# Kernel tuning notes

Measured on AMD Instinct MI355X. Metric: run time of the kernel, lower is better.

## Reference

```python
import jax, jax.numpy as jnp
import numpy as np

B, CIN, IMG, PATCH = 4, 1, 64, 8
SIDE = IMG // PATCH            # 8
N = SIDE ** 3                  # 512 tokens
C = 384
HEADS, HD = 6, 64
IFF = 1536
WS, SHIFT = 2, 1
NB = 4                         # 4 dense blocks + 4 shifted-window blocks (8 layers)
NKP = 15
EPS = 1e-5


def _ln(x, g, b):
    m = x.mean(-1, keepdims=True)
    v = ((x - m) ** 2).mean(-1, keepdims=True)
    return (x - m) * jax.lax.rsqrt(v + EPS) * g + b


def _mhsa(x, qw, kw, vw, pw, pb):
    # per-head Q/K/V linears (no bias), stacked as [H, C, HD]
    q = jnp.einsum('bnc,hcd->bhnd', x, qw)
    k = jnp.einsum('bnc,hcd->bhnd', x, kw)
    v = jnp.einsum('bnc,hcd->bhnd', x, vw)
    a = jax.nn.softmax(jnp.einsum('bhnd,bhmd->bhnm', q, k) / np.float32(np.sqrt(HD)), axis=-1)
    o = jnp.einsum('bhnm,bhmd->bhnd', a, v)
    o = o.transpose(0, 2, 1, 3).reshape(x.shape[0], x.shape[1], C)
    return o @ pw + pb


def _swin_attn(x, qkv_w, qkv_b, pw, pb):
    Bn = x.shape[0]
    H = W = D = SIDE
    xv = x.transpose(0, 2, 1).reshape(Bn, C, H, W, D)
    xv = jnp.roll(xv, (-SHIFT, -SHIFT, -SHIFT), axis=(2, 3, 4))
    # window partition -> [Bn*nw^3, WS^3, C]
    xv = xv.reshape(Bn, C, H // WS, WS, W // WS, WS, D // WS, WS)
    win = xv.transpose(0, 2, 4, 6, 3, 5, 7, 1).reshape(-1, WS ** 3, C)
    qkv = win @ qkv_w + qkv_b                                      # [Bw, ws3, 3C]
    qkv = qkv.reshape(win.shape[0], WS ** 3, 3, HEADS, HD).transpose(2, 0, 3, 1, 4)
    q, k, v = qkv[0], qkv[1], qkv[2]
    a = jax.nn.softmax(jnp.einsum('whnd,whmd->whnm', q, k) / np.float32(np.sqrt(HD)), axis=-1)
    o = jnp.einsum('whnm,whmd->whnd', a, v)
    o = o.transpose(0, 2, 1, 3).reshape(win.shape[0], WS ** 3, C)
    o = o @ pw + pb
    # window reverse
    o = o.reshape(Bn, H // WS, W // WS, D // WS, WS, WS, WS, C)
    o = o.transpose(0, 7, 1, 4, 2, 5, 3, 6).reshape(Bn, C, H, W, D)
    o = jnp.roll(o, (SHIFT, SHIFT, SHIFT), axis=(2, 3, 4))
    return o.reshape(Bn, C, -1).transpose(0, 2, 1)


def _ffn(x, w1, b1, w2, b2):
    return jax.nn.relu(x @ w1 + b1) @ w2 + b2


def _deconv2(x, w, b):
    # ConvTranspose3d kernel=stride=2 (no overlap): pure block upsample GEMM
    Bn, Cc, H, W, D = x.shape
    O = w.shape[1]
    y = jnp.einsum('bchwd,coijk->bohiwjdk', x, w)
    return y.reshape(Bn, O, 2 * H, 2 * W, 2 * D) + b[None, :, None, None, None]


def _bn_relu(x, g, b, m, v):
    sh = (1, -1, 1, 1, 1)
    y = (x - m.reshape(sh)) * jax.lax.rsqrt(v.reshape(sh) + EPS) * g.reshape(sh) + b.reshape(sh)
    return jax.nn.relu(y)


def setup_inputs() -> dict:
    key = jax.random.key(0)
    ks = iter(jax.random.split(key, 40))
    nrm = lambda shape, s=0.02: jax.random.normal(next(ks), shape, jnp.float32) * s
    inp = {
        'x': jax.random.normal(next(ks), (B, CIN, IMG, IMG, IMG), jnp.float32),
        'patch_w': nrm((C, CIN, PATCH, PATCH, PATCH)),
        'patch_b': jnp.zeros((C,), jnp.float32),
        'pos_emb': nrm((1, N, C)),
        # 4 dense blocks (stacked)
        'm_ln1_g': jnp.ones((NB, C)), 'm_ln1_b': jnp.zeros((NB, C)),
        'm_qw': nrm((NB, HEADS, C, HD)), 'm_kw': nrm((NB, HEADS, C, HD)), 'm_vw': nrm((NB, HEADS, C, HD)),
        'm_proj_w': nrm((NB, C, C)), 'm_proj_b': jnp.zeros((NB, C)),
        'm_ln2_g': jnp.ones((NB, C)), 'm_ln2_b': jnp.zeros((NB, C)),
        'm_w1': nrm((NB, C, IFF)), 'm_b1': jnp.zeros((NB, IFF)),
        'm_w2': nrm((NB, IFF, C)), 'm_b2': jnp.zeros((NB, C)),
        # 4 shifted-window blocks (stacked)
        's_ln1_g': jnp.ones((NB, C)), 's_ln1_b': jnp.zeros((NB, C)),
        's_qkv_w': nrm((NB, C, 3 * C)), 's_qkv_b': jnp.zeros((NB, 3 * C)),
        's_proj_w': nrm((NB, C, C)), 's_proj_b': jnp.zeros((NB, C)),
        's_ln2_g': jnp.ones((NB, C)), 's_ln2_b': jnp.zeros((NB, C)),
        's_w1': nrm((NB, C, IFF)), 's_b1': jnp.zeros((NB, IFF)),
        's_w2': nrm((NB, IFF, C)), 's_b2': jnp.zeros((NB, C)),
        # ClassicDecoder
        'd1_w': nrm((C, C, 2, 2, 2)), 'd1_b': jnp.zeros((C,)),
        'bn1_g': jnp.ones((C,)), 'bn1_b': jnp.zeros((C,)), 'bn1_m': jnp.zeros((C,)), 'bn1_v': jnp.ones((C,)),
        'd2_w': nrm((C, C, 2, 2, 2)), 'd2_b': jnp.zeros((C,)),
        'bn2_g': jnp.ones((C,)), 'bn2_b': jnp.zeros((C,)), 'bn2_m': jnp.zeros((C,)), 'bn2_v': jnp.ones((C,)),
        'out_w': nrm((NKP, C)), 'out_b': jnp.zeros((NKP,)),
    }
    return inp


def reference(x, patch_w, patch_b, pos_emb,
              m_ln1_g, m_ln1_b, m_qw, m_kw, m_vw, m_proj_w, m_proj_b,
              m_ln2_g, m_ln2_b, m_w1, m_b1, m_w2, m_b2,
              s_ln1_g, s_ln1_b, s_qkv_w, s_qkv_b, s_proj_w, s_proj_b,
              s_ln2_g, s_ln2_b, s_w1, s_b1, s_w2, s_b2,
              d1_w, d1_b, bn1_g, bn1_b, bn1_m, bn1_v,
              d2_w, d2_b, bn2_g, bn2_b, bn2_m, bn2_v,
              out_w, out_b):
    # patch embedding: Conv3d(k=stride=patch) -> [B, N, C]
    t = jax.lax.conv_general_dilated(x, patch_w, (PATCH, PATCH, PATCH), 'VALID',
                                     dimension_numbers=('NCDHW', 'OIDHW', 'NCDHW'))
    t = t + patch_b[None, :, None, None, None]
    t = t.reshape(B, C, N).transpose(0, 2, 1) + pos_emb
    for i in range(2 * NB):
        j = i // 2
        if i % 2 == 0:  # dense Block
            t = t + _mhsa(_ln(t, m_ln1_g[j], m_ln1_b[j]), m_qw[j], m_kw[j], m_vw[j], m_proj_w[j], m_proj_b[j])
            t = t + _ffn(_ln(t, m_ln2_g[j], m_ln2_b[j]), m_w1[j], m_b1[j], m_w2[j], m_b2[j])
        else:           # ShiftedWindowBlock
            t = t + _swin_attn(_ln(t, s_ln1_g[j], s_ln1_b[j]), s_qkv_w[j], s_qkv_b[j], s_proj_w[j], s_proj_b[j])
            t = t + _ffn(_ln(t, s_ln2_g[j], s_ln2_b[j]), s_w1[j], s_b1[j], s_w2[j], s_b2[j])
    # ClassicDecoder
    y = t.transpose(0, 2, 1).reshape(B, C, SIDE, SIDE, SIDE)
    y = _bn_relu(_deconv2(y, d1_w, d1_b), bn1_g, bn1_b, bn1_m, bn1_v)
    y = _bn_relu(_deconv2(y, d2_w, d2_b), bn2_g, bn2_b, bn2_m, bn2_v)
    y = jnp.einsum('bchwd,oc->bohwd', y, out_w) + out_b[None, :, None, None, None]
    return y
```

## Files before the change

kernel.cpp:

```cpp
#include <hip/hip_runtime.h>
#include <hip/hip_bf16.h>


typedef unsigned short u16;
typedef __bf16 bf16x8 __attribute__((ext_vector_type(8)));
typedef float f32x4 __attribute__((ext_vector_type(4)));

__device__ __forceinline__ u16 f2bf(float f) {
  unsigned u = __builtin_bit_cast(unsigned, f);
  return (u16)((u + 0x7FFFu + ((u >> 16) & 1u)) >> 16);
}
__device__ __forceinline__ float bf2f(u16 b) {
  unsigned u = ((unsigned)b) << 16;
  return __builtin_bit_cast(float, u);
}

#define GLOAD_LDS16(g, l)                                                      \
  __builtin_amdgcn_global_load_lds(                                            \
      (const __attribute__((address_space(1))) unsigned int*)(const void*)(g), \
      (__attribute__((address_space(3))) unsigned int*)(void*)(l), 16, 0, 0)

struct MmP {
  const u16* A;
  const u16* Bt;
  const float* bias;
  void* C;
  void* aux;
  const float* e1; const float* e2; const float* e3; const float* e4;
  int K, ZH, lda, ldb, ldc;
  long aSb, aSh, bSb, bSh, cSb, cSh;
};

template<int MODE, int BM>
__global__ __launch_bounds__(256) void mfma_gemm(MmP p) {
  const int z = blockIdx.z;
  const int zb = z / p.ZH, zh = z - zb * p.ZH;
  const u16* A  = p.A  + zb * p.aSb + zh * p.aSh;
  const u16* Bt = p.Bt + zb * p.bSb + zh * p.bSh;
  const int m0 = blockIdx.y * BM, n0 = blockIdx.x * 64;

  __shared__ u16 As[2][BM * 64];
  __shared__ u16 Bs[2][64 * 64];

  const int tid = threadIdx.x;
  const int wid = tid >> 6, lane = tid & 63;
  constexpr int MI = BM / 32;
  const int wm = (wid >> 1) * (BM / 2), wn = (wid & 1) * 32;
  const int lr = lane & 15, lg = lane >> 4;
  constexpr int ACH = BM / 32;

  f32x4 acc[MI][2];
  #pragma unroll
  for (int i = 0; i < MI; i++)
    #pragma unroll
    for (int j = 0; j < 2; j++) acc[i][j] = (f32x4){0.f, 0.f, 0.f, 0.f};

  auto stage = [&](int buf, int kt) {
    #pragma unroll
    for (int i = 0; i < ACH; i++) {
      int c = i * 256 + tid;
      int row = c >> 3, cc = c & 7;
      int gk = ((cc ^ (row & 7)) << 3) + (kt << 6);
      GLOAD_LDS16(A + (long)(m0 + row) * p.lda + gk, As[buf] + c * 8);
    }
    #pragma unroll
    for (int i = 0; i < 2; i++) {
      int c = i * 256 + tid;
      int row = c >> 3, cc = c & 7;
      int gk = ((cc ^ (row & 7)) << 3) + (kt << 6);
      GLOAD_LDS16(Bt + (long)(n0 + row) * p.ldb + gk, Bs[buf] + c * 8);
    }
  };

  const int nKT = p.K >> 6;
  stage(0, 0);
  asm volatile("s_waitcnt vmcnt(0)");
  __syncthreads();

  int cur = 0;
  for (int kt = 0; kt < nKT; ++kt) {
    const bool more = (kt + 1 < nKT);
    if (more) stage(cur ^ 1, kt + 1);

    bf16x8 af[MI][2], bfr[2][2];
    #pragma unroll
    for (int i = 0; i < MI; i++)
      #pragma unroll
      for (int ks = 0; ks < 2; ks++) {
        int row = wm + i * 16 + lr;
        int j = ks * 4 + lg;
        af[i][ks] = *(const bf16x8*)(As[cur] + (row * 8 + (j ^ (row & 7))) * 8);
      }
    #pragma unroll
    for (int jn = 0; jn < 2; jn++)
      #pragma unroll
      for (int ks = 0; ks < 2; ks++) {
        int row = wn + jn * 16 + lr;
        int j = ks * 4 + lg;
        bfr[jn][ks] = *(const bf16x8*)(Bs[cur] + (row * 8 + (j ^ (row & 7))) * 8);
      }
    #pragma unroll
    for (int i = 0; i < MI; i++)
      #pragma unroll
      for (int jn = 0; jn < 2; jn++)
        #pragma unroll
        for (int ks = 0; ks < 2; ks++)
          acc[i][jn] = __builtin_amdgcn_mfma_f32_16x16x32_bf16(
              af[i][ks], bfr[jn][ks], acc[i][jn], 0, 0, 0);

    if (more) {
      asm volatile("s_waitcnt vmcnt(0)");
      __syncthreads();
      cur ^= 1;
    }
  }

  const long coff = zb * p.cSb + zh * p.cSh;
  #pragma unroll
  for (int i = 0; i < MI; i++) {
    const int rowb = m0 + wm + i * 16 + lg * 4;
    #pragma unroll
    for (int jn = 0; jn < 2; jn++) {
      const int col = n0 + wn + jn * 16 + lr;
      const float bv = p.bias ? p.bias[col] : 0.f;
      #pragma unroll
      for (int r = 0; r < 4; r++) {
        const int row = rowb + r;
        const float v = acc[i][jn][r];
        if constexpr (MODE == 0) {
          ((u16*)p.C)[coff + (long)row * p.ldc + col] = f2bf(v + bv);
        } else if constexpr (MODE == 1) {
          ((float*)p.C)[coff + (long)row * p.ldc + col] =
              v + bv + p.e1[(long)(row & 511) * 384 + col];
        } else if constexpr (MODE == 2) {
          ((float*)p.C)[coff + (long)row * p.ldc + col] += v + bv;
        } else if constexpr (MODE == 3) {
          ((u16*)p.C)[coff + (long)row * p.ldc + col] = f2bf(fmaxf(v + bv, 0.f));
        } else if constexpr (MODE == 5) {
          float raw = v + bv;
          float val = fmaxf((raw - p.e3[col]) * rsqrtf(p.e4[col] + 1e-5f) * p.e1[col] + p.e2[col], 0.f);
          int b = row >> 9, hwd = row & 511;
          int h = hwd >> 6, w = (hwd >> 3) & 7, d = hwd & 7;
          int i_ = zh >> 2, j_ = (zh >> 1) & 1, k_ = zh & 1;
          long tokn = (long)b * 4096 + (2 * h + i_) * 256 + (2 * w + j_) * 16 + (2 * d + k_);
          ((u16*)p.C)[tokn * 384 + col] = f2bf(val);
        } else if constexpr (MODE == 6) {
          float raw = v + bv;
          float val = fmaxf((raw - p.e3[col]) * rsqrtf(p.e4[col] + 1e-5f) * p.e1[col] + p.e2[col], 0.f);
          ((u16*)p.C)[(long)row * p.ldc + col] = f2bf(val);
        } else if constexpr (MODE == 7) {
          u16 bv16 = f2bf(v);
          ((u16*)p.C)[coff + (long)row * p.ldc + col] = bv16;
          if (col >= 768) {
            int bb = row >> 9, tt = row & 511;
            int hh = (col - 768) >> 6, dd = col & 63;
            ((u16*)p.aux)[(((long)bb * 6 + hh) << 15) + (dd << 9) + tt] = bv16;
          }
        }
      }
    }
  }
}

__global__ __launch_bounds__(512) void attnsm_k(const u16* __restrict__ qkv, u16* __restrict__ P) {
  const int bh = blockIdx.y;
  const int b = bh / 6, h = bh - b * 6;
  const int qt = blockIdx.x;
  const int tid = threadIdx.x, wid = tid >> 6, lane = tid & 63;
  const int lr = lane & 15, lg = lane >> 4;
  __shared__ u16 Ks[512 * 64];
  const u16* qbase = qkv + ((long)b * 512) * 1152 + h * 64;

  #pragma unroll
  for (int i = 0; i < 8; i++) {
    int c = i * 512 + tid;
    int t = c >> 3, cc = c & 7;
    int gk = (cc ^ (t & 7)) << 3;
    GLOAD_LDS16(qbase + (long)t * 1152 + 384 + gk, Ks + c * 8);
  }
  const int qrow = qt * 128 + wid * 16 + lr;
  bf16x8 qf[2];
  #pragma unroll
  for (int ks = 0; ks < 2; ks++)
    qf[ks] = *(const bf16x8*)(qbase + (long)qrow * 1152 + (ks * 4 + lg) * 8);
  asm volatile("s_waitcnt vmcnt(0)");
  __syncthreads();

  f32x4 s[32];
  #pragma unroll
  for (int nt = 0; nt < 32; nt++) {
    s[nt] = (f32x4){0.f, 0.f, 0.f, 0.f};
    #pragma unroll
    for (int ks = 0; ks < 2; ks++) {
      int row = nt * 16 + lr;
      int j = ks * 4 + lg;
      bf16x8 kf = *(const bf16x8*)(Ks + (row * 8 + (j ^ (row & 7))) * 8);
      s[nt] = __builtin_amdgcn_mfma_f32_16x16x32_bf16(qf[ks], kf, s[nt], 0, 0, 0);
    }
  }
  float mx[4] = {-1e30f, -1e30f, -1e30f, -1e30f};
  #pragma unroll
  for (int nt = 0; nt < 32; nt++)
    #pragma unroll
    for (int r = 0; r < 4; r++) { s[nt][r] *= 0.125f; mx[r] = fmaxf(mx[r], s[nt][r]); }
  #pragma unroll
  for (int o = 8; o >= 1; o >>= 1)
    #pragma unroll
    for (int r = 0; r < 4; r++) mx[r] = fmaxf(mx[r], __shfl_xor(mx[r], o));
  float sum[4] = {0.f, 0.f, 0.f, 0.f};
  #pragma unroll
  for (int nt = 0; nt < 32; nt++)
    #pragma unroll
    for (int r = 0; r < 4; r++) { float e = __expf(s[nt][r] - mx[r]); s[nt][r] = e; sum[r] += e; }
  #pragma unroll
  for (int o = 8; o >= 1; o >>= 1)
    #pragma unroll
    for (int r = 0; r < 4; r++) sum[r] += __shfl_xor(sum[r], o);
  float inv[4];
  #pragma unroll
  for (int r = 0; r < 4; r++) inv[r] = 1.f / sum[r];

  u16* Pb = P + (long)bh * 262144;
  const int prow0 = qt * 128 + wid * 16 + lg * 4;
  #pragma unroll
  for (int nt = 0; nt < 32; nt++)
    #pragma unroll
    for (int r = 0; r < 4; r++)
      Pb[(long)(prow0 + r) * 512 + nt * 16 + lr] = f2bf(s[nt][r] * inv[r]);
}


__global__ __launch_bounds__(256) void ln_k(const float* __restrict__ x, const float* __restrict__ g,
                                            const float* __restrict__ b, u16* __restrict__ y) {
  const int row = (blockIdx.x << 2) + (threadIdx.x >> 6);
  const int lane = threadIdx.x & 63;
  const float* xr = x + (long)row * 384;
  float v[6]; float s = 0.f;
  #pragma unroll
  for (int i = 0; i < 6; i++) { v[i] = xr[lane + (i << 6)]; s += v[i]; }
  #pragma unroll
  for (int o = 32; o >= 1; o >>= 1) s += __shfl_xor(s, o);
  const float mean = s * (1.f / 384.f);
  float q = 0.f;
  #pragma unroll
  for (int i = 0; i < 6; i++) { float dd = v[i] - mean; q += dd * dd; }
  #pragma unroll
  for (int o = 32; o >= 1; o >>= 1) q += __shfl_xor(q, o);
  const float rstd = rsqrtf(q * (1.f / 384.f) + 1e-5f);
  u16* yr = y + (long)row * 384;
  #pragma unroll
  for (int i = 0; i < 6; i++) {
    int c = lane + (i << 6);
    yr[c] = f2bf((v[i] - mean) * rstd * g[c] + b[c]);
  }
}

__global__ __launch_bounds__(64) void swin_k(const u16* __restrict__ qkv, u16* __restrict__ attno) {
  const int blk = blockIdx.x;
  const int h = blk % 6; const int bw = blk / 6;
  const int b = bw >> 6, win = bw & 63;
  const int wh = win >> 4, ww = (win >> 2) & 3, wd = win & 3;
  const int lane = threadIdx.x;
  __shared__ float qs[8][68], ks[8][68], vs[8][68], attw[8][8];
  __shared__ int ntok[8];
  if (lane < 8) {
    int i = lane >> 2, j = (lane >> 1) & 1, k = lane & 1;
    int oh = (2 * wh + i + 1) & 7, ow = (2 * ww + j + 1) & 7, od = (2 * wd + k + 1) & 7;
    ntok[lane] = oh * 64 + ow * 8 + od;
  }
  __syncthreads();
  #pragma unroll
  for (int t = 0; t < 8; t++) {
    long base = ((long)b * 512 + ntok[t]) * 1152 + h * 64 + lane;
    qs[t][lane] = bf2f(qkv[base]);
    ks[t][lane] = bf2f(qkv[base + 384]);
    vs[t][lane] = bf2f(qkv[base + 768]);
  }
  __syncthreads();
  const int tq = lane >> 3, tm = lane & 7;
  float sc = 0.f;
  #pragma unroll 16
  for (int d = 0; d < 64; d++) sc += qs[tq][d] * ks[tm][d];
  sc *= 0.125f;
  float mx = sc;
  mx = fmaxf(mx, __shfl_xor(mx, 4));
  mx = fmaxf(mx, __shfl_xor(mx, 2));
  mx = fmaxf(mx, __shfl_xor(mx, 1));
  float e = __expf(sc - mx);
  float sm = e;
  sm += __shfl_xor(sm, 4); sm += __shfl_xor(sm, 2); sm += __shfl_xor(sm, 1);
  attw[tq][tm] = e / sm;
  __syncthreads();
  #pragma unroll
  for (int t = 0; t < 8; t++) {
    float o = 0.f;
    #pragma unroll
    for (int m = 0; m < 8; m++) o += attw[t][m] * vs[m][lane];
    attno[((long)b * 512 + ntok[t]) * 384 + h * 64 + lane] = f2bf(o);
  }
}

__global__ __launch_bounds__(256) void im2col_k(const float* __restrict__ x, u16* __restrict__ xp) {
  const int i = blockIdx.x * 256 + threadIdx.x;
  const int l = i & 511; const int m = i >> 9;
  const int b = m >> 9, n = m & 511;
  const int h = n >> 6, w = (n >> 3) & 7, d = n & 7;
  const int pi = l >> 6, pj = (l >> 3) & 7, pk = l & 7;
  xp[i] = f2bf(x[(long)b * 262144 + (long)(h * 8 + pi) * 4096 + (w * 8 + pj) * 64 + (d * 8 + pk)]);
}

__global__ __launch_bounds__(256) void castw_k(const float* __restrict__ in, u16* __restrict__ out, int n) {
  for (int i = blockIdx.x * 256 + threadIdx.x; i < n; i += gridDim.x * 256)
    out[i] = f2bf(in[i]);
}

struct TJ { const float* s[7]; u16* d[7]; };
__global__ __launch_bounds__(256) void transpose_tiled_k(TJ tj) {
  __shared__ u16 tile[64][65];
  const int cumt[8] = {0, 432, 576, 720, 1296, 1872, 2448, 3024};
  const int bi = blockIdx.x;
  int j = 0;
  #pragma unroll
  for (int t = 1; t < 7; t++) if (bi >= cumt[t]) j = t;
  const int li = bi - cumt[j];
  const int Kj = (j >= 5) ? 1536 : 384;
  const int Nj = (j == 0) ? 1152 : ((j == 3 || j == 4) ? 1536 : 384);
  const int tn_cnt = Nj >> 6;
  const int per_z = (Kj >> 6) * tn_cnt;
  const int z = li / per_z;
  int rem = li - z * per_z;
  const int tk = rem / tn_cnt, tn = rem - tk * tn_cnt;
  const float* src = tj.s[j] + (long)z * Kj * Nj;
  u16* dst = tj.d[j] + (long)z * Kj * Nj;
  const int k0 = tk << 6, n0 = tn << 6;
  const int rl = threadIdx.x >> 6, c = threadIdx.x & 63;
  #pragma unroll
  for (int i = 0; i < 16; i++) {
    int r = i * 4 + rl;
    tile[r][c] = f2bf(src[(long)(k0 + r) * Nj + n0 + c]);
  }
  __syncthreads();
  #pragma unroll
  for (int i = 0; i < 16; i++) {
    int n = i * 4 + rl;
    dst[(long)(n0 + n) * Kj + k0 + c] = tile[c][n];
  }
}

__global__ __launch_bounds__(256) void repack_mqkv_k2(const float* __restrict__ qw, const float* __restrict__ kw,
                                                      const float* __restrict__ vw, u16* __restrict__ out) {
  __shared__ u16 tile[64][65];
  const int bi = blockIdx.x;
  const int j = bi / 108;
  int rem = bi - j * 108;
  const int s = rem / 36; rem -= s * 36;
  const int h = rem / 6, tk = rem - h * 6;
  const float* src = (s == 0 ? qw : s == 1 ? kw : vw) + (long)j * 147456;
  const int rl = threadIdx.x >> 6, cc = threadIdx.x & 63;
  #pragma unroll
  for (int i = 0; i < 16; i++) {
    int cl = tk * 64 + i * 4 + rl;
    tile[i * 4 + rl][cc] = f2bf(src[(long)(h * 384 + cl) * 64 + cc]);
  }
  __syncthreads();
  u16* ob = out + (long)j * 442368 + (long)(s * 384 + h * 64) * 384 + tk * 64;
  #pragma unroll
  for (int i = 0; i < 16; i++) {
    int d = i * 4 + rl;
    ob[(long)d * 384 + cc] = tile[cc][d];
  }
}

__global__ __launch_bounds__(256) void repack_dw_k2(const float* __restrict__ in, u16* __restrict__ out) {
  __shared__ u16 ds[32][514];
  const int bo = blockIdx.x % 6, bc = blockIdx.x / 6;
  const int c0 = bc * 32, o0 = bo * 64;
  #pragma unroll 4
  for (int it = 0; it < 64; it++) {
    int fl = it * 256 + threadIdx.x;
    int cr = fl >> 9, mm = fl & 511;
    ds[cr][mm] = f2bf(in[(long)(c0 + cr) * 3072 + o0 * 8 + mm]);
  }
  __syncthreads();
  #pragma unroll 4
  for (int it = 0; it < 64; it++) {
    int fl = it * 256 + threadIdx.x;
    int ijk = fl >> 11, rem = fl & 2047;
    int oo = rem >> 5, cr = rem & 31;
    out[(long)ijk * 147456 + (long)(o0 + oo) * 384 + c0 + cr] = ds[cr][oo * 8 + ijk];
  }
}

__global__ __launch_bounds__(256) void contract_k(const u16* __restrict__ act, const float* __restrict__ ow,
                                                  const float* __restrict__ ob, float* __restrict__ out, int ijk) {
  __shared__ __align__(16) float tile[16][388];
  __shared__ __align__(16) float wsh[15][388];
  const int tid = threadIdx.x;
  for (int idx = tid; idx < 15 * 384; idx += 256) {
    int kp = idx / 384, c = idx - kp * 384;
    wsh[kp][c] = ow[idx];
  }
  const long row0 = (long)blockIdx.x << 4;
  for (int idx = tid; idx < 16 * 384; idx += 256) {
    int r = idx / 384, c = idx - r * 384;
    tile[r][c] = bf2f(act[(row0 + r) * 384 + c]);
  }
  __syncthreads();
  const int r = tid >> 4, kp = tid & 15;
  if (kp < 15) {
    float acc = 0.f;
    #pragma unroll 8
    for (int c = 0; c < 384; c += 4) {
      float4 a = *(const float4*)&tile[r][c];
      float4 w = *(const float4*)&wsh[kp][c];
      acc += a.x * w.x + a.y * w.y + a.z * w.z + a.w * w.w;
    }
    const int gm = (int)row0 + r;
    const int b = gm >> 12, h = (gm >> 8) & 15, w = (gm >> 4) & 15, d = gm & 15;
    const int i = ijk >> 2, j = (ijk >> 1) & 1, k = ijk & 1;
    const long o = ((long)(b * 15 + kp) << 15) + (2 * h + i) * 1024 + (2 * w + j) * 32 + (2 * d + k);
    out[o] = acc + ob[kp];
  }
}


static MmP mk(const u16* A, const u16* Bt, const float* bias, void* C,
              int K, int lda, int ldb, int ldc) {
  MmP p{};
  p.A = A; p.Bt = Bt; p.bias = bias; p.C = C; p.aux = nullptr;
  p.e1 = p.e2 = p.e3 = p.e4 = nullptr;
  p.K = K; p.ZH = 1; p.lda = lda; p.ldb = ldb; p.ldc = ldc;
  p.aSb = p.aSh = p.bSb = p.bSh = p.cSb = p.cSh = 0;
  return p;
}

extern "C" void kernel_launch(void* const* d_in, const int* in_sizes, int n_in,
                              void* d_out, int out_size, void* d_ws, size_t ws_size,
                              hipStream_t stream) {
  (void)in_sizes; (void)n_in; (void)out_size; (void)ws_size;
  const float* x        = (const float*)d_in[0];
  const float* patch_w  = (const float*)d_in[1];
  const float* patch_b  = (const float*)d_in[2];
  const float* pos_emb  = (const float*)d_in[3];
  const float* m_ln1_g  = (const float*)d_in[4];
  const float* m_ln1_b  = (const float*)d_in[5];
  const float* m_qw     = (const float*)d_in[6];
  const float* m_kw     = (const float*)d_in[7];
  const float* m_vw     = (const float*)d_in[8];
  const float* m_proj_w = (const float*)d_in[9];
  const float* m_proj_b = (const float*)d_in[10];
  const float* m_ln2_g  = (const float*)d_in[11];
  const float* m_ln2_b  = (const float*)d_in[12];
  const float* m_w1     = (const float*)d_in[13];
  const float* m_b1     = (const float*)d_in[14];
  const float* m_w2     = (const float*)d_in[15];
  const float* m_b2     = (const float*)d_in[16];
  const float* s_ln1_g  = (const float*)d_in[17];
  const float* s_ln1_b  = (const float*)d_in[18];
  const float* s_qkv_w  = (const float*)d_in[19];
  const float* s_qkv_b  = (const float*)d_in[20];
  const float* s_proj_w = (const float*)d_in[21];
  const float* s_proj_b = (const float*)d_in[22];
  const float* s_ln2_g  = (const float*)d_in[23];
  const float* s_ln2_b  = (const float*)d_in[24];
  const float* s_w1     = (const float*)d_in[25];
  const float* s_b1     = (const float*)d_in[26];
  const float* s_w2     = (const float*)d_in[27];
  const float* s_b2     = (const float*)d_in[28];
  const float* d1_w     = (const float*)d_in[29];
  const float* d1_b     = (const float*)d_in[30];
  const float* bn1_g    = (const float*)d_in[31];
  const float* bn1_b    = (const float*)d_in[32];
  const float* bn1_m    = (const float*)d_in[33];
  const float* bn1_v    = (const float*)d_in[34];
  const float* d2_w     = (const float*)d_in[35];
  const float* d2_b     = (const float*)d_in[36];
  const float* bn2_g    = (const float*)d_in[37];
  const float* bn2_b    = (const float*)d_in[38];
  const float* bn2_m    = (const float*)d_in[39];
  const float* bn2_v    = (const float*)d_in[40];
  const float* out_w    = (const float*)d_in[41];
  const float* out_b    = (const float*)d_in[42];
  float* out = (float*)d_out;

  char* wsp = (char*)d_ws;
  auto alloc = [&](size_t bytes) { void* p = wsp; wsp += (bytes + 255) & ~(size_t)255; return p; };
  float* tok    = (float*)alloc(786432 * 4);
  u16* wqkv_m   = (u16*)alloc(1769472 * 2);
  u16* wqkv_s   = (u16*)alloc(1769472 * 2);
  u16* wproj_m  = (u16*)alloc(589824 * 2);
  u16* wproj_s  = (u16*)alloc(589824 * 2);
  u16* w1m      = (u16*)alloc(2359296 * 2);
  u16* w1s      = (u16*)alloc(2359296 * 2);
  u16* w2m      = (u16*)alloc(2359296 * 2);
  u16* w2s      = (u16*)alloc(2359296 * 2);
  u16* wpatch   = (u16*)alloc(196608 * 2);
  u16* wd1      = (u16*)alloc(1179648 * 2);
  u16* wd2      = (u16*)alloc(1179648 * 2);
  u16* lnb      = (u16*)alloc(786432 * 2);
  u16* qkvb     = (u16*)alloc(2359296 * 2);
  u16* attnob   = (u16*)alloc(786432 * 2);
  u16* ffnhb    = (u16*)alloc(3145728 * 2);
  u16* scoresb  = (u16*)alloc(6291456 * 2);
  u16* vTb      = (u16*)alloc(786432 * 2);
  u16* xpb   = scoresb;
  u16* y1b   = scoresb;
  u16* out2b = qkvb;
  u16* tokb  = vTb;

  castw_k<<<256, 256, 0, stream>>>(patch_w, wpatch, 196608);
  repack_mqkv_k2<<<432, 256, 0, stream>>>(m_qw, m_kw, m_vw, wqkv_m);
  {
    TJ tj;
    tj.s[0] = s_qkv_w;  tj.d[0] = wqkv_s;
    tj.s[1] = m_proj_w; tj.d[1] = wproj_m;
    tj.s[2] = s_proj_w; tj.d[2] = wproj_s;
    tj.s[3] = m_w1;     tj.d[3] = w1m;
    tj.s[4] = s_w1;     tj.d[4] = w1s;
    tj.s[5] = m_w2;     tj.d[5] = w2m;
    tj.s[6] = s_w2;     tj.d[6] = w2s;
    transpose_tiled_k<<<3024, 256, 0, stream>>>(tj);
  }
  repack_dw_k2<<<72, 256, 0, stream>>>(d1_w, wd1);
  repack_dw_k2<<<72, 256, 0, stream>>>(d2_w, wd2);

  im2col_k<<<4096, 256, 0, stream>>>(x, xpb);
  {
    MmP p = mk(xpb, wpatch, patch_b, tok, 512, 512, 512, 384);
    p.e1 = pos_emb;
    mfma_gemm<1, 64><<<dim3(6, 32, 1), 256, 0, stream>>>(p);
  }

  for (int j = 0; j < 4; j++) {
    ln_k<<<512, 256, 0, stream>>>(tok, m_ln1_g + j * 384, m_ln1_b + j * 384, lnb);
    {
      MmP p = mk(lnb, wqkv_m + (long)j * 442368, nullptr, qkvb, 384, 384, 384, 1152);
      p.aux = vTb;
      mfma_gemm<7, 128><<<dim3(18, 16, 1), 256, 0, stream>>>(p);
    }
    attnsm_k<<<dim3(4, 24, 1), 512, 0, stream>>>(qkvb, scoresb);
    {
      MmP p = mk(scoresb, vTb, nullptr, attnob, 512, 512, 512, 384);
      p.ZH = 6; p.aSb = 1572864; p.aSh = 262144; p.bSb = 196608; p.bSh = 32768;
      p.cSb = 196608; p.cSh = 64;
      mfma_gemm<0, 64><<<dim3(1, 8, 24), 256, 0, stream>>>(p);
    }
    {
      MmP p = mk(attnob, wproj_m + (long)j * 147456, m_proj_b + j * 384, tok, 384, 384, 384, 384);
      mfma_gemm<2, 64><<<dim3(6, 32, 1), 256, 0, stream>>>(p);
    }
    ln_k<<<512, 256, 0, stream>>>(tok, m_ln2_g + j * 384, m_ln2_b + j * 384, lnb);
    {
      MmP p = mk(lnb, w1m + (long)j * 589824, m_b1 + j * 1536, ffnhb, 384, 384, 384, 1536);
      mfma_gemm<3, 128><<<dim3(24, 16, 1), 256, 0, stream>>>(p);
    }
    {
      MmP p = mk(ffnhb, w2m + (long)j * 589824, m_b2 + j * 384, tok, 1536, 1536, 1536, 384);
      mfma_gemm<2, 64><<<dim3(6, 32, 1), 256, 0, stream>>>(p);
    }

    ln_k<<<512, 256, 0, stream>>>(tok, s_ln1_g + j * 384, s_ln1_b + j * 384, lnb);
    {
      MmP p = mk(lnb, wqkv_s + (long)j * 442368, s_qkv_b + j * 1152, qkvb, 384, 384, 384, 1152);
      mfma_gemm<0, 128><<<dim3(18, 16, 1), 256, 0, stream>>>(p);
    }
    swin_k<<<1536, 64, 0, stream>>>(qkvb, attnob);
    {
      MmP p = mk(attnob, wproj_s + (long)j * 147456, s_proj_b + j * 384, tok, 384, 384, 384, 384);
      mfma_gemm<2, 64><<<dim3(6, 32, 1), 256, 0, stream>>>(p);
    }
    ln_k<<<512, 256, 0, stream>>>(tok, s_ln2_g + j * 384, s_ln2_b + j * 384, lnb);
    {
      MmP p = mk(lnb, w1s + (long)j * 589824, s_b1 + j * 1536, ffnhb, 384, 384, 384, 1536);
      mfma_gemm<3, 128><<<dim3(24, 16, 1), 256, 0, stream>>>(p);
    }
    {
      MmP p = mk(ffnhb, w2s + (long)j * 589824, s_b2 + j * 384, tok, 1536, 1536, 1536, 384);
      mfma_gemm<2, 64><<<dim3(6, 32, 1), 256, 0, stream>>>(p);
    }
  }

  castw_k<<<768, 256, 0, stream>>>(tok, tokb, 786432);
  {
    MmP p = mk(tokb, wd1, d1_b, y1b, 384, 384, 384, 384);
    p.ZH = 8; p.bSh = 147456;
    p.e1 = bn1_g; p.e2 = bn1_b; p.e3 = bn1_m; p.e4 = bn1_v;
    mfma_gemm<5, 128><<<dim3(6, 16, 8), 256, 0, stream>>>(p);
  }
  for (int ijk = 0; ijk < 8; ijk++) {
    {
      MmP p = mk(y1b, wd2 + (long)ijk * 147456, d2_b, out2b, 384, 384, 384, 384);
      p.e1 = bn2_g; p.e2 = bn2_b; p.e3 = bn2_m; p.e4 = bn2_v;
      mfma_gemm<6, 128><<<dim3(6, 128, 1), 256, 0, stream>>>(p);
    }
    contract_k<<<1024, 256, 0, stream>>>(out2b, out_w, out_b, out, ijk);
  }
}
```

Measured before the change: 1.066 ms.

## Fuse second deconv GEMM, BN-ReLU and output projection into one kernel

Replaces the per-offset loop of deconv2 GEMM plus a separate 1x1 output contraction with a single kernel covering all eight offsets. Each 64-row tile runs the MFMA GEMM, applies bias, BN and ReLU, keeps the bf16 result in LDS and contracts it with the 15-channel output weights directly. This removes 16 launches and the round trip of the large intermediate activation through global memory, at the cost of heavy LDS use per block. It also shrinks the attention softmax block to 256 threads with twice as many blocks, and merges the two decoder weight repack launches.

```diff
diff --git a/kernel.cpp b/kernel.cpp
--- a/kernel.cpp
+++ b/kernel.cpp
@@ -4,6 +4,7 @@
 
 typedef unsigned short u16;
 typedef __bf16 bf16x8 __attribute__((ext_vector_type(8)));
+typedef unsigned short u16x8 __attribute__((ext_vector_type(8)));
 typedef float f32x4 __attribute__((ext_vector_type(4)));
 
 __device__ __forceinline__ u16 f2bf(float f) {
@@ -144,10 +145,6 @@
           int i_ = zh >> 2, j_ = (zh >> 1) & 1, k_ = zh & 1;
           long tokn = (long)b * 4096 + (2 * h + i_) * 256 + (2 * w + j_) * 16 + (2 * d + k_);
           ((u16*)p.C)[tokn * 384 + col] = f2bf(val);
-        } else if constexpr (MODE == 6) {
-          float raw = v + bv;
-          float val = fmaxf((raw - p.e3[col]) * rsqrtf(p.e4[col] + 1e-5f) * p.e1[col] + p.e2[col], 0.f);
-          ((u16*)p.C)[(long)row * p.ldc + col] = f2bf(val);
         } else if constexpr (MODE == 7) {
           u16 bv16 = f2bf(v);
           ((u16*)p.C)[coff + (long)row * p.ldc + col] = bv16;
@@ -162,7 +159,131 @@
   }
 }
 
-__global__ __launch_bounds__(512) void attnsm_k(const u16* __restrict__ qkv, u16* __restrict__ P) {
+__global__ __launch_bounds__(512) void dc2_k(const u16* __restrict__ y1, const u16* __restrict__ wd2,
+                                             const float* __restrict__ d2b,
+                                             const float* __restrict__ g, const float* __restrict__ bta,
+                                             const float* __restrict__ mu, const float* __restrict__ var,
+                                             const float* __restrict__ ow, const float* __restrict__ ob,
+                                             float* __restrict__ out) {
+  __shared__ char smem[114688];
+  u16* As = (u16*)smem;
+  u16* Bs = (u16*)(smem + 16384);
+  u16* H2 = (u16*)(smem + 16384);
+  float* ows = (float*)(smem + 16384 + 50176);
+
+  const int ijk = blockIdx.y;
+  const int m0 = blockIdx.x * 64;
+  const u16* Bt = wd2 + (long)ijk * 147456;
+  const int tid = threadIdx.x;
+  const int wid = tid >> 6, lane = tid & 63;
+  const int wr = wid >> 2, wc = wid & 3;
+  const int lr = lane & 15, lg = lane >> 4;
+
+  f32x4 acc[2][6];
+  #pragma unroll
+  for (int i = 0; i < 2; i++)
+    #pragma unroll
+    for (int j = 0; j < 6; j++) acc[i][j] = (f32x4){0.f, 0.f, 0.f, 0.f};
+
+  auto stage = [&](int buf, int kt) {
+    {
+      int c = tid;
+      int row = c >> 3, cc = c & 7;
+      int gk = ((cc ^ (row & 7)) << 3) + (kt << 6);
+      GLOAD_LDS16(y1 + (long)(m0 + row) * 384 + gk, As + buf * 4096 + c * 8);
+    }
+    #pragma unroll
+    for (int i = 0; i < 6; i++) {
+      int c = i * 512 + tid;
+      int row = c >> 3, cc = c & 7;
+      int gk = ((cc ^ (row & 7)) << 3) + (kt << 6);
+      GLOAD_LDS16(Bt + (long)row * 384 + gk, Bs + buf * 24576 + c * 8);
+    }
+  };
+  stage(0, 0);
+  asm volatile("s_waitcnt vmcnt(0)");
+  __syncthreads();
+  int cur = 0;
+  for (int kt = 0; kt < 6; ++kt) {
+    const bool more = (kt < 5);
+    if (more) stage(cur ^ 1, kt + 1);
+    bf16x8 af[2][2], bfr[6][2];
+    #pragma unroll
+    for (int i = 0; i < 2; i++)
+      #pragma unroll
+      for (int ks = 0; ks < 2; ks++) {
+        int row = wr * 32 + i * 16 + lr;
+        int j = ks * 4 + lg;
+        af[i][ks] = *(const bf16x8*)(As + cur * 4096 + (row * 8 + (j ^ (row & 7))) * 8);
+      }
+    #pragma unroll
+    for (int jn = 0; jn < 6; jn++)
+      #pragma unroll
+      for (int ks = 0; ks < 2; ks++) {
+        int row = wc * 96 + jn * 16 + lr;
+        int j = ks * 4 + lg;
+        bfr[jn][ks] = *(const bf16x8*)(Bs + cur * 24576 + (row * 8 + (j ^ (row & 7))) * 8);
+      }
+    #pragma unroll
+    for (int i = 0; i < 2; i++)
+      #pragma unroll
+      for (int jn = 0; jn < 6; jn++)
+        #pragma unroll
+        for (int ks = 0; ks < 2; ks++)
+          acc[i][jn] = __builtin_amdgcn_mfma_f32_16x16x32_bf16(
+              af[i][ks], bfr[jn][ks], acc[i][jn], 0, 0, 0);
+    if (more) {
+      asm volatile("s_waitcnt vmcnt(0)");
+      __syncthreads();
+      cur ^= 1;
+    }
+  }
+  __syncthreads();
+
+  #pragma unroll
+  for (int i = 0; i < 2; i++)
+    #pragma unroll
+    for (int jn = 0; jn < 6; jn++) {
+      const int col = wc * 96 + jn * 16 + lr;
+      const float scale = rsqrtf(var[col] + 1e-5f) * g[col];
+      const float bias2 = bta[col] - mu[col] * scale;
+      const float db = d2b[col];
+      #pragma unroll
+      for (int r = 0; r < 4; r++) {
+        int row = wr * 32 + i * 16 + lg * 4 + r;
+        float val = fmaxf((acc[i][jn][r] + db) * scale + bias2, 0.f);
+        H2[row * 392 + col] = f2bf(val);
+      }
+    }
+  for (int idx = tid; idx < 15 * 384; idx += 512) {
+    int kp = idx / 384, c = idx - kp * 384;
+    ows[kp * 388 + c] = ow[idx];
+  }
+  __syncthreads();
+
+  const int kp = tid & 15, rbase = tid >> 4;
+  if (kp < 15) {
+    const int i_ = ijk >> 2, j_ = (ijk >> 1) & 1, k_ = ijk & 1;
+    #pragma unroll
+    for (int pass = 0; pass < 2; pass++) {
+      const int r = rbase + pass * 32;
+      float a = 0.f;
+      #pragma unroll 4
+      for (int c = 0; c < 384; c += 8) {
+        u16x8 hv = *(const u16x8*)&H2[r * 392 + c];
+        const float* wp = &ows[kp * 388 + c];
+        #pragma unroll
+        for (int u = 0; u < 8; u++) a += bf2f(hv[u]) * wp[u];
+      }
+      const int gm = m0 + r;
+      const int b = gm >> 12, h = (gm >> 8) & 15, w = (gm >> 4) & 15, d = gm & 15;
+      const long o = ((long)(b * 15 + kp) << 15) + (2 * h + i_) * 1024 + (2 * w + j_) * 32 + (2 * d + k_);
+      out[o] = a + ob[kp];
+    }
+  }
+}
+
+__global__ __launch_bounds__(256) void attnsm_k(const u16* __restrict__ qkv, u16* __restrict__ P) {
   const int bh = blockIdx.y;
   const int b = bh / 6, h = bh - b * 6;
   const int qt = blockIdx.x;
@@ -172,13 +293,13 @@
   const u16* qbase = qkv + ((long)b * 512) * 1152 + h * 64;
 
   #pragma unroll
-  for (int i = 0; i < 8; i++) {
-    int c = i * 512 + tid;
+  for (int i = 0; i < 16; i++) {
+    int c = i * 256 + tid;
     int t = c >> 3, cc = c & 7;
     int gk = (cc ^ (t & 7)) << 3;
     GLOAD_LDS16(qbase + (long)t * 1152 + 384 + gk, Ks + c * 8);
   }
-  const int qrow = qt * 128 + wid * 16 + lr;
+  const int qrow = qt * 64 + wid * 16 + lr;
   bf16x8 qf[2];
   #pragma unroll
   for (int ks = 0; ks < 2; ks++)
@@ -221,7 +342,7 @@
   for (int r = 0; r < 4; r++) inv[r] = 1.f / sum[r];
 
   u16* Pb = P + (long)bh * 262144;
-  const int prow0 = qt * 128 + wid * 16 + lg * 4;
+  const int prow0 = qt * 64 + wid * 16 + lg * 4;
   #pragma unroll
   for (int nt = 0; nt < 32; nt++)
     #pragma unroll
@@ -371,9 +492,14 @@
   }
 }
 
-__global__ __launch_bounds__(256) void repack_dw_k2(const float* __restrict__ in, u16* __restrict__ out) {
+__global__ __launch_bounds__(256) void repack_dw2_k(const float* __restrict__ in1, u16* __restrict__ out1,
+                                                    const float* __restrict__ in2, u16* __restrict__ out2) {
   __shared__ u16 ds[32][514];
-  const int bo = blockIdx.x % 6, bc = blockIdx.x / 6;
+  const int sel = blockIdx.x >= 72;
+  const float* in = sel ? in2 : in1;
+  u16* out = sel ? out2 : out1;
+  const int bx = sel ? blockIdx.x - 72 : blockIdx.x;
+  const int bo = bx % 6, bc = bx / 6;
   const int c0 = bc * 32, o0 = bo * 64;
   #pragma unroll 4
   for (int it = 0; it < 64; it++) {
@@ -388,38 +514,6 @@
     int ijk = fl >> 11, rem = fl & 2047;
     int oo = rem >> 5, cr = rem & 31;
     out[(long)ijk * 147456 + (long)(o0 + oo) * 384 + c0 + cr] = ds[cr][oo * 8 + ijk];
-  }
-}
-
-__global__ __launch_bounds__(256) void contract_k(const u16* __restrict__ act, const float* __restrict__ ow,
-                                                  const float* __restrict__ ob, float* __restrict__ out, int ijk) {
-  __shared__ __align__(16) float tile[16][388];
-  __shared__ __align__(16) float wsh[15][388];
-  const int tid = threadIdx.x;
-  for (int idx = tid; idx < 15 * 384; idx += 256) {
-    int kp = idx / 384, c = idx - kp * 384;
-    wsh[kp][c] = ow[idx];
-  }
-  const long row0 = (long)blockIdx.x << 4;
-  for (int idx = tid; idx < 16 * 384; idx += 256) {
-    int r = idx / 384, c = idx - r * 384;
-    tile[r][c] = bf2f(act[(row0 + r) * 384 + c]);
-  }
-  __syncthreads();
-  const int r = tid >> 4, kp = tid & 15;
-  if (kp < 15) {
-    float acc = 0.f;
-    #pragma unroll 8
-    for (int c = 0; c < 384; c += 4) {
-      float4 a = *(const float4*)&tile[r][c];
-      float4 w = *(const float4*)&wsh[kp][c];
-      acc += a.x * w.x + a.y * w.y + a.z * w.z + a.w * w.w;
-    }
-    const int gm = (int)row0 + r;
-    const int b = gm >> 12, h = (gm >> 8) & 15, w = (gm >> 4) & 15, d = gm & 15;
-    const int i = ijk >> 2, j = (ijk >> 1) & 1, k = ijk & 1;
-    const long o = ((long)(b * 15 + kp) << 15) + (2 * h + i) * 1024 + (2 * w + j) * 32 + (2 * d + k);
-    out[o] = acc + ob[kp];
   }
 }
 
@@ -505,7 +599,6 @@
   u16* vTb      = (u16*)alloc(786432 * 2);
   u16* xpb   = scoresb;
   u16* y1b   = scoresb;
-  u16* out2b = qkvb;
   u16* tokb  = vTb;
 
   castw_k<<<256, 256, 0, stream>>>(patch_w, wpatch, 196608);
@@ -521,8 +614,7 @@
     tj.s[6] = s_w2;     tj.d[6] = w2s;
     transpose_tiled_k<<<3024, 256, 0, stream>>>(tj);
   }
-  repack_dw_k2<<<72, 256, 0, stream>>>(d1_w, wd1);
-  repack_dw_k2<<<72, 256, 0, stream>>>(d2_w, wd2);
+  repack_dw2_k<<<144, 256, 0, stream>>>(d1_w, wd1, d2_w, wd2);
 
   im2col_k<<<4096, 256, 0, stream>>>(x, xpb);
   {
@@ -538,7 +630,7 @@
       p.aux = vTb;
       mfma_gemm<7, 128><<<dim3(18, 16, 1), 256, 0, stream>>>(p);
     }
-    attnsm_k<<<dim3(4, 24, 1), 512, 0, stream>>>(qkvb, scoresb);
+    attnsm_k<<<dim3(8, 24, 1), 256, 0, stream>>>(qkvb, scoresb);
     {
       MmP p = mk(scoresb, vTb, nullptr, attnob, 512, 512, 512, 384);
       p.ZH = 6; p.aSb = 1572864; p.aSh = 262144; p.bSb = 196608; p.bSh = 32768;
@@ -587,12 +679,6 @@
     p.e1 = bn1_g; p.e2 = bn1_b; p.e3 = bn1_m; p.e4 = bn1_v;
     mfma_gemm<5, 128><<<dim3(6, 16, 8), 256, 0, stream>>>(p);
   }
-  for (int ijk = 0; ijk < 8; ijk++) {
-    {
-      MmP p = mk(y1b, wd2 + (long)ijk * 147456, d2_b, out2b, 384, 384, 384, 384);
-      p.e1 = bn2_g; p.e2 = bn2_b; p.e3 = bn2_m; p.e4 = bn2_v;
-      mfma_gemm<6, 128><<<dim3(6, 128, 1), 256, 0, stream>>>(p);
-    }
-    contract_k<<<1024, 256, 0, stream>>>(out2b, out_w, out_b, out, ijk);
-  }
-}
+  dc2_k<<<dim3(256, 8, 1), 512, 0, stream>>>(y1b, wd2, d2_b, bn2_g, bn2_b, bn2_m, bn2_v,
+                                             out_w, out_b, out);
+}
```

After: 960.1 us. 9.9% less time.
